# Performance work log

Hardware: AMD Instinct MI355X
Metric: run time of the kernel (lower is better)

The kernel has to match this reference:

```python
import jax, jax.numpy as jnp
import numpy as np

N_NODES = 100000
N_EDGES = 1600000
D_IN, D_HID, D_OUT = 64, 128, 64


def setup_inputs() -> dict:
    key = jax.random.key(0)
    ks = jax.random.split(key, 12)
    s = lambda d: 1.0 / np.sqrt(d)
    return {
        "x": jax.random.normal(ks[0], (N_NODES, D_IN), dtype=jnp.float32),
        "edge_index": jax.random.randint(ks[1], (2, N_EDGES), 0, N_NODES, dtype=jnp.int64),
        # conv1 MLP: Linear(D_IN->D_HID), ReLU, Linear(D_HID->D_HID)
        "W1a": jax.random.uniform(ks[2], (D_IN, D_HID), jnp.float32, -s(D_IN), s(D_IN)),
        "b1a": jnp.zeros((D_HID,), jnp.float32),
        "W1b": jax.random.uniform(ks[3], (D_HID, D_HID), jnp.float32, -s(D_HID), s(D_HID)),
        "b1b": jnp.zeros((D_HID,), jnp.float32),
        # conv2 MLP: Linear(D_HID->D_HID), ReLU, Linear(D_HID->D_HID)
        "W2a": jax.random.uniform(ks[4], (D_HID, D_HID), jnp.float32, -s(D_HID), s(D_HID)),
        "b2a": jnp.zeros((D_HID,), jnp.float32),
        "W2b": jax.random.uniform(ks[5], (D_HID, D_HID), jnp.float32, -s(D_HID), s(D_HID)),
        "b2b": jnp.zeros((D_HID,), jnp.float32),
        # final projection Linear(D_HID->D_OUT)
        "Wlin": jax.random.uniform(ks[6], (D_HID, D_OUT), jnp.float32, -s(D_HID), s(D_HID)),
        "blin": jnp.zeros((D_OUT,), jnp.float32),
    }


def _gin_conv(h, src, dst, Wa, ba, Wb, bb, num_nodes):
    # GINConv (eps=0): MLP((1+eps)*x + sum_{j->i} x_j)
    agg = jax.ops.segment_sum(h[src], dst, num_segments=num_nodes)  # [N, d]
    z = h + agg
    z = jax.nn.relu(z @ Wa + ba)
    return z @ Wb + bb


def reference(x, edge_index, W1a, b1a, W1b, b1b, W2a, b2a, W2b, b2b, Wlin, blin):
    n = x.shape[0]
    src, dst = edge_index[0], edge_index[1]
    h = jax.nn.relu(_gin_conv(x, src, dst, W1a, b1a, W1b, b1b, n))
    h = jax.nn.relu(_gin_conv(h, src, dst, W2a, b2a, W2b, b2b, n))
    return h @ Wlin + blin  # [N, D_OUT]
```

## Files before the change

### kernel.cpp

```cpp
#include <hip/hip_runtime.h>
#include <hip/hip_fp16.h>


typedef __attribute__((ext_vector_type(8))) short short8;
typedef __attribute__((ext_vector_type(8))) _Float16 half8;
typedef __attribute__((ext_vector_type(4))) float f32x4;
union F8 { unsigned u[4]; uint4 u4; short8 s; half8 h; };


constexpr int BUCKET_SHIFT = 9;
constexpr int BUCKET_NODES = 1 << BUCKET_SHIFT;
constexpr int CAP = 10240;
constexpr int EPB = 2048;
constexpr int NBUCK_MAX = 256;

__global__ __launch_bounds__(256) void prep_scatter_kernel(const int* __restrict__ ei, int E,
                                                           int* __restrict__ gcur,
                                                           int* __restrict__ gpk,
                                                           int nbuck, int nbs,
                                                           const float* __restrict__ W1a,
                                                           const float* __restrict__ W1b,
                                                           const float* __restrict__ W2a,
                                                           const float* __restrict__ W2b,
                                                           const float* __restrict__ Wlin,
                                                           short* __restrict__ hi,
                                                           const float* __restrict__ x,
                                                           __half2* __restrict__ x16, int n2,
                                                           int npb) {
    __shared__ int spk[EPB];
    __shared__ unsigned char sbuck[EPB];
    __shared__ int lcnt[NBUCK_MAX];
    __shared__ int lbase[NBUCK_MAX];
    __shared__ int lcur[NBUCK_MAX];
    __shared__ int gbase[NBUCK_MAX];
    __shared__ int stmp[256];

    const int t = threadIdx.x;

    if (blockIdx.x >= nbs) {
        int pb = blockIdx.x - nbs;
        int i = pb * 256 + t;
        if (i < 65536) {
            const float* W;
            int base, K, N;
            if (i < 8192)       { W = W1a;  base = 0;     K = 64;  N = 128; }
            else if (i < 24576) { W = W1b;  base = 8192;  K = 128; N = 128; }
            else if (i < 40960) { W = W2a;  base = 24576; K = 128; N = 128; }
            else if (i < 57344) { W = W2b;  base = 40960; K = 128; N = 128; }
            else                { W = Wlin; base = 57344; K = 128; N = 64;  }
            int rel = i - base;
            int NT = N >> 4;
            int j  = rel & 7;
            int l  = (rel >> 3) & 63;
            int tc = rel >> 9;
            int nt = tc % NT;
            int c  = tc / NT;
            int n  = nt * 16 + (l & 15);
            int k  = c * 32 + ((l >> 4) << 3) + j;
            float v = W[k * N + n];
            hi[i] = (short)__half_as_ushort(__float2half_rn(v));
        }
        for (int k = i; k < n2; k += npb * 256) {
            float2 v = reinterpret_cast<const float2*>(x)[k];
            x16[k] = __floats2half2_rn(v.x, v.y);
        }
        return;
    }

    const int e0 = blockIdx.x * EPB;
    const int ecnt = min(EPB, E - e0);

    for (int i = t; i < NBUCK_MAX; i += 256) lcnt[i] = 0;
    __syncthreads();

    for (int i = t; i < ecnt; i += 256) {
        int d = ei[E + e0 + i];
        atomicAdd(&lcnt[d >> BUCKET_SHIFT], 1);
    }
    __syncthreads();

    int v = lcnt[t];
    stmp[t] = v;
    __syncthreads();
    #pragma unroll
    for (int off = 1; off < 256; off <<= 1) {
        int add = (t >= off) ? stmp[t - off] : 0;
        __syncthreads();
        stmp[t] += add;
        __syncthreads();
    }
    lbase[t] = stmp[t] - v;
    lcur[t] = stmp[t] - v;
    __syncthreads();

    for (int i = t; i < ecnt; i += 256) {
        int s = ei[e0 + i];
        int d = ei[E + e0 + i];
        int b = d >> BUCKET_SHIFT;
        int p = atomicAdd(&lcur[b], 1);
        spk[p] = ((d & (BUCKET_NODES - 1)) << 17) | s;
        sbuck[p] = (unsigned char)b;
    }
    __syncthreads();

    if (t < nbuck) {
        int c = lcnt[t];
        gbase[t] = (c > 0) ? atomicAdd(&gcur[t], c) : 0;
    }
    __syncthreads();

    for (int i = t; i < ecnt; i += 256) {
        int b = sbuck[i];
        int gp = gbase[b] + (i - lbase[b]);
        if (gp < CAP) gpk[(size_t)b * CAP + gp] = spk[i];
    }
}

__global__ __launch_bounds__(1024) void bucket_build_kernel(const int* __restrict__ gpk,
                                                            const int* __restrict__ gcur,
                                                            int* __restrict__ row_start,
                                                            int* __restrict__ edge_src,
                                                            int N, int E, int nbuck) {
    __shared__ int h[BUCKET_NODES];
    __shared__ int s[BUCKET_NODES];
    __shared__ int sb[NBUCK_MAX];
    __shared__ int bbase_sh;
    const int t = threadIdx.x;
    const int b = blockIdx.x;
    const int base = b << BUCKET_SHIFT;

    if (t < NBUCK_MAX) {
        int c = 0;
        if (t < nbuck) c = min(gcur[t], CAP);
        sb[t] = c;
    }
    for (int i = t; i < BUCKET_NODES; i += 1024) h[i] = 0;
    __syncthreads();
    #pragma unroll
    for (int off = 1; off < NBUCK_MAX; off <<= 1) {
        int add = (t >= off && t < NBUCK_MAX) ? sb[t - off] : 0;
        __syncthreads();
        if (t < NBUCK_MAX) sb[t] += add;
        __syncthreads();
    }
    if (t == 0) {
        int cb0 = min(gcur[b], CAP);
        bbase_sh = sb[b] - cb0;
    }

    int cb = min(gcur[b], CAP);
    const int* pp = gpk + (size_t)b * CAP;
    for (int i = t; i < cb; i += 1024) atomicAdd(&h[((unsigned)pp[i]) >> 17], 1);
    __syncthreads();

    int c0 = (t < BUCKET_NODES) ? h[t] : 0;
    if (t < BUCKET_NODES) s[t] = c0;
    __syncthreads();
    #pragma unroll
    for (int off = 1; off < BUCKET_NODES; off <<= 1) {
        int add = (t >= off && t < BUCKET_NODES) ? s[t - off] : 0;
        __syncthreads();
        if (t < BUCKET_NODES) s[t] += add;
        __syncthreads();
    }
    if (t < BUCKET_NODES) {
        int ex = s[t] - c0 + bbase_sh;
        h[t] = ex;
        if (base + t < N) row_start[base + t] = ex;
    }
    if (b == 0 && t == 0) row_start[N] = E;
    __syncthreads();

    for (int i = t; i < cb; i += 1024) {
        unsigned pw = (unsigned)pp[i];
        int p = atomicAdd(&h[pw >> 17], 1);
        edge_src[p] = (int)(pw & 0x1FFFFu);
    }
}


__device__ inline void acc8(float* a, const uint4& v) {
    const __half2* h = reinterpret_cast<const __half2*>(&v);
    #pragma unroll
    for (int j = 0; j < 4; ++j) {
        float2 f = __half22float2(h[j]);
        a[2 * j]     += f.x;
        a[2 * j + 1] += f.y;
    }
}

__device__ inline uint4 pack8(const float* a) {
    uint4 o;
    __half2 h;
    h = __floats2half2_rn(a[0], a[1]); o.x = *reinterpret_cast<unsigned*>(&h);
    h = __floats2half2_rn(a[2], a[3]); o.y = *reinterpret_cast<unsigned*>(&h);
    h = __floats2half2_rn(a[4], a[5]); o.z = *reinterpret_cast<unsigned*>(&h);
    h = __floats2half2_rn(a[6], a[7]); o.w = *reinterpret_cast<unsigned*>(&h);
    return o;
}

__global__ __launch_bounds__(256) void agg128_fp16(const __half2* __restrict__ H16,
                                                   const int* __restrict__ row_start,
                                                   const int* __restrict__ edge_src,
                                                   __half2* __restrict__ Z16, int N) {
    int wave = threadIdx.x >> 6, lane = threadIdx.x & 63;
    int node = blockIdx.x * 4 + wave;
    if (node >= N) return;
    const int lg = lane >> 4;
    const int lo = lane & 15;
    const uint4* Hv = reinterpret_cast<const uint4*>(H16);
    int beg = row_start[node], end = row_start[node + 1];

    uint4 selfv = Hv[(size_t)node * 16 + lo];

    float a[8];
    #pragma unroll
    for (int j = 0; j < 8; ++j) a[j] = 0.f;
    if (lg == 0) acc8(a, selfv);

    int i = beg;
    for (; i + 16 <= end; i += 16) {
        int s0 = edge_src[i + lg];
        int s1 = edge_src[i + 4 + lg];
        int s2 = edge_src[i + 8 + lg];
        int s3 = edge_src[i + 12 + lg];
        uint4 v0 = Hv[(size_t)s0 * 16 + lo];
        uint4 v1 = Hv[(size_t)s1 * 16 + lo];
        uint4 v2 = Hv[(size_t)s2 * 16 + lo];
        uint4 v3 = Hv[(size_t)s3 * 16 + lo];
        acc8(a, v0); acc8(a, v1); acc8(a, v2); acc8(a, v3);
    }
    if (i + 8 <= end) {
        int s0 = edge_src[i + lg];
        int s1 = edge_src[i + 4 + lg];
        uint4 v0 = Hv[(size_t)s0 * 16 + lo];
        uint4 v1 = Hv[(size_t)s1 * 16 + lo];
        acc8(a, v0); acc8(a, v1);
        i += 8;
    }
    if (i + 4 <= end) {
        int s0 = edge_src[i + lg];
        uint4 v0 = Hv[(size_t)s0 * 16 + lo];
        acc8(a, v0);
        i += 4;
    }
    int rem = end - i;
    if (lg < rem) {
        int s0 = edge_src[i + lg];
        uint4 v0 = Hv[(size_t)s0 * 16 + lo];
        acc8(a, v0);
    }

    #pragma unroll
    for (int j = 0; j < 8; ++j) {
        a[j] += __shfl_xor(a[j], 16);
        a[j] += __shfl_xor(a[j], 32);
    }

    if (lg == 0) {
        reinterpret_cast<uint4*>(Z16)[(size_t)node * 16 + lo] = pack8(a);
    }
}

__global__ __launch_bounds__(256) void agg64_fp16(const __half2* __restrict__ H16,
                                                  const int* __restrict__ row_start,
                                                  const int* __restrict__ edge_src,
                                                  __half2* __restrict__ Z16, int N) {
    int wave = threadIdx.x >> 6, lane = threadIdx.x & 63;
    int node = blockIdx.x * 4 + wave;
    if (node >= N) return;
    const int lg = lane >> 3;
    const int lo = lane & 7;
    const uint4* Hv = reinterpret_cast<const uint4*>(H16);
    int beg = row_start[node], end = row_start[node + 1];

    uint4 selfv = Hv[(size_t)node * 8 + lo];

    float a[8];
    #pragma unroll
    for (int j = 0; j < 8; ++j) a[j] = 0.f;
    if (lg == 0) acc8(a, selfv);

    int i = beg;
    for (; i + 16 <= end; i += 16) {
        int s0 = edge_src[i + lg];
        int s1 = edge_src[i + 8 + lg];
        uint4 v0 = Hv[(size_t)s0 * 8 + lo];
        uint4 v1 = Hv[(size_t)s1 * 8 + lo];
        acc8(a, v0); acc8(a, v1);
    }
    if (i + 8 <= end) {
        int s0 = edge_src[i + lg];
        uint4 v0 = Hv[(size_t)s0 * 8 + lo];
        acc8(a, v0);
        i += 8;
    }
    int rem = end - i;
    if (lg < rem) {
        int s0 = edge_src[i + lg];
        uint4 v0 = Hv[(size_t)s0 * 8 + lo];
        acc8(a, v0);
    }

    #pragma unroll
    for (int j = 0; j < 8; ++j) {
        a[j] += __shfl_xor(a[j], 8);
        a[j] += __shfl_xor(a[j], 16);
        a[j] += __shfl_xor(a[j], 32);
    }

    if (lg == 0) {
        reinterpret_cast<uint4*>(Z16)[(size_t)node * 8 + lo] = pack8(a);
    }
}


template <int K, int NT>
__device__ inline void compute_directA(const __half2* __restrict__ z, int M, int m0,
                                       const short* __restrict__ WH,
                                       int w, int lane, f32x4 (*acc)[8]) {
    constexpr int KC = K / 32;
    const short8* bhp = reinterpret_cast<const short8*>(WH) + lane;
    const int q = lane >> 4, ln = lane & 15;
    const uint4* zr[2];
    #pragma unroll
    for (int mt = 0; mt < 2; ++mt) {
        int row = m0 + (w * 2 + mt) * 16 + ln;
        if (row >= M) row = M - 1;
        zr[mt] = reinterpret_cast<const uint4*>(z + (size_t)row * (K / 2));
    }
    for (int c = 0; c < KC; ++c) {
        F8 bh[NT];
        #pragma unroll
        for (int nt = 0; nt < NT; ++nt) bh[nt].s = bhp[(c * NT + nt) * 64];
        #pragma unroll
        for (int mt = 0; mt < 2; ++mt) {
            F8 ah;
            ah.u4 = zr[mt][c * 4 + q];
            #pragma unroll
            for (int nt = 0; nt < NT; ++nt) {
                acc[mt][nt] = __builtin_amdgcn_mfma_f32_16x16x32_f16(ah.h, bh[nt].h, acc[mt][nt], 0, 0, 0);
            }
        }
    }
}

template <int K, int NT>
__device__ inline void stage_compute(const unsigned* __restrict__ P,
                                     const short* __restrict__ WH,
                                     int w, int lane, f32x4 (*acc)[8]) {
    constexpr int KC = K / 32;
    const short8* bhp = reinterpret_cast<const short8*>(WH) + lane;
    for (int c = 0; c < KC; ++c) {
        F8 bh[NT];
        #pragma unroll
        for (int nt = 0; nt < NT; ++nt) {
            bh[nt].s = bhp[(c * NT + nt) * 64];
        }
        #pragma unroll
        for (int mt = 0; mt < 2; ++mt) {
            const int T = w * 2 + mt;
            const unsigned* Pb = P + ((T * KC + c) * 8) * 66 + lane;
            unsigned d[8];
            #pragma unroll
            for (int j = 0; j < 8; ++j) d[j] = Pb[j * 66];
            F8 ah;
            #pragma unroll
            for (int j = 0; j < 4; ++j) {
                ah.u[j] = __builtin_amdgcn_perm(d[2 * j + 1], d[2 * j], 0x05040100u);
            }
            #pragma unroll
            for (int nt = 0; nt < NT; ++nt) {
                acc[mt][nt] = __builtin_amdgcn_mfma_f32_16x16x32_f16(ah.h, bh[nt].h, acc[mt][nt], 0, 0, 0);
            }
        }
    }
}

__device__ inline void epilogue_tile(const f32x4* acc, const float* __restrict__ bias,
                                     unsigned* __restrict__ Pout, int T, int lane) {
    int q = lane >> 4, ln = lane & 15;
    #pragma unroll
    for (int nt = 0; nt < 8; ++nt) {
        int col = nt * 16 + ln;
        float b = bias[col];
        int c = col >> 5, jj = col & 7, q2 = (col >> 3) & 3;
        int pb = ((T * 4 + c) * 8 + jj) * 66;
        #pragma unroll
        for (int r = 0; r < 4; ++r) {
            float v = fmaxf(acc[nt][r] + b, 0.f);
            Pout[pb + ((q * 4 + r) | (q2 << 4))] =
                (unsigned)__half_as_ushort(__float2half_rn(v));
        }
    }
}

__global__ __launch_bounds__(256, 2) void mfma_mlp_A(const __half2* __restrict__ z16,
                                                     const short* __restrict__ WaH,
                                                     const float* __restrict__ ba,
                                                     const short* __restrict__ WbH,
                                                     const float* __restrict__ bb,
                                                     __half* __restrict__ H16out, int M) {
    __shared__ unsigned P[8 * 4 * 8 * 66];
    const int t = threadIdx.x;
    const int w = t >> 6, lane = t & 63;
    const int m0 = blockIdx.x * 128;
    const int q = lane >> 4, ln = lane & 15;

    f32x4 acc[2][8];
    #pragma unroll
    for (int mt = 0; mt < 2; ++mt)
        #pragma unroll
        for (int i = 0; i < 8; ++i) acc[mt][i] = (f32x4){0.f, 0.f, 0.f, 0.f};
    compute_directA<64, 8>(z16, M, m0, WaH, w, lane, acc);
    epilogue_tile(acc[0], ba, P, w * 2 + 0, lane);
    epilogue_tile(acc[1], ba, P, w * 2 + 1, lane);

    #pragma unroll
    for (int mt = 0; mt < 2; ++mt)
        #pragma unroll
        for (int i = 0; i < 8; ++i) acc[mt][i] = (f32x4){0.f, 0.f, 0.f, 0.f};
    stage_compute<128, 8>(P, WbH, w, lane, acc);

    #pragma unroll
    for (int mt = 0; mt < 2; ++mt) {
        #pragma unroll
        for (int nt = 0; nt < 8; ++nt) {
            int col = nt * 16 + ln;
            float b = bb[col];
            #pragma unroll
            for (int r = 0; r < 4; ++r) {
                int row = m0 + (w * 2 + mt) * 16 + q * 4 + r;
                if (row < M) {
                    float v = fmaxf(acc[mt][nt][r] + b, 0.f);
                    H16out[(size_t)row * 128 + col] = __float2half_rn(v);
                }
            }
        }
    }
}

__global__ __launch_bounds__(256, 2) void mfma_mlp_B(const __half2* __restrict__ z16,
                                                     const short* __restrict__ WaH,
                                                     const float* __restrict__ ba,
                                                     const short* __restrict__ WbH,
                                                     const float* __restrict__ bb,
                                                     const short* __restrict__ WlH,
                                                     const float* __restrict__ bl,
                                                     float* __restrict__ Out, int M) {
    __shared__ unsigned P[8 * 4 * 8 * 66];
    const int t = threadIdx.x;
    const int w = t >> 6, lane = t & 63;
    const int m0 = blockIdx.x * 128;
    const int q = lane >> 4, ln = lane & 15;

    f32x4 acc[2][8];
    #pragma unroll
    for (int mt = 0; mt < 2; ++mt)
        #pragma unroll
        for (int i = 0; i < 8; ++i) acc[mt][i] = (f32x4){0.f, 0.f, 0.f, 0.f};
    compute_directA<128, 8>(z16, M, m0, WaH, w, lane, acc);
    epilogue_tile(acc[0], ba, P, w * 2 + 0, lane);
    epilogue_tile(acc[1], ba, P, w * 2 + 1, lane);

    #pragma unroll
    for (int mt = 0; mt < 2; ++mt)
        #pragma unroll
        for (int i = 0; i < 8; ++i) acc[mt][i] = (f32x4){0.f, 0.f, 0.f, 0.f};
    stage_compute<128, 8>(P, WbH, w, lane, acc);
    epilogue_tile(acc[0], bb, P, w * 2 + 0, lane);
    epilogue_tile(acc[1], bb, P, w * 2 + 1, lane);

    #pragma unroll
    for (int mt = 0; mt < 2; ++mt)
        #pragma unroll
        for (int i = 0; i < 8; ++i) acc[mt][i] = (f32x4){0.f, 0.f, 0.f, 0.f};
    stage_compute<128, 4>(P, WlH, w, lane, acc);

    #pragma unroll
    for (int mt = 0; mt < 2; ++mt) {
        #pragma unroll
        for (int nt = 0; nt < 4; ++nt) {
            int col = nt * 16 + ln;
            float b = bl[col];
            #pragma unroll
            for (int r = 0; r < 4; ++r) {
                int row = m0 + (w * 2 + mt) * 16 + q * 4 + r;
                if (row < M) Out[(size_t)row * 64 + col] = acc[mt][nt][r] + b;
            }
        }
    }
}


extern "C" void kernel_launch(void* const* d_in, const int* in_sizes, int n_in,
                              void* d_out, int out_size, void* d_ws, size_t ws_size,
                              hipStream_t stream) {
    const float* x    = (const float*)d_in[0];
    const int*   ei   = (const int*)d_in[1];
    const float* W1a  = (const float*)d_in[2];
    const float* b1a  = (const float*)d_in[3];
    const float* W1b  = (const float*)d_in[4];
    const float* b1b  = (const float*)d_in[5];
    const float* W2a  = (const float*)d_in[6];
    const float* b2a  = (const float*)d_in[7];
    const float* W2b  = (const float*)d_in[8];
    const float* b2b  = (const float*)d_in[9];
    const float* Wlin = (const float*)d_in[10];
    const float* blin = (const float*)d_in[11];
    float* out = (float*)d_out;

    const int N = in_sizes[0] / 64;
    const int E = in_sizes[1] / 2;
    const int NBUCK = (N + BUCKET_NODES - 1) >> BUCKET_SHIFT;

    char* ws = (char*)d_ws;
    const size_t bufBytes = (size_t)N * 128 * sizeof(float);
    __half2* Zbuf = (__half2*)(ws + 0);
    char* B = ws + bufBytes;
    size_t off = 3 * bufBytes;
    int* row_start = (int*)(ws + off); off += ((size_t)(N + 1) * 4 + 15) & ~(size_t)15;
    int* cnt       = (int*)(ws + off); off += ((size_t)N * 4 + 15) & ~(size_t)15;
    int* partials  = (int*)(ws + off); off += 4096;
    int* gcur      = (int*)(ws + off); off += 4096;
    int* edge_src  = (int*)(ws + off); off += (size_t)E * 4;
    __half* h116   = (__half*)(ws + off); off += (size_t)N * 128 * 2;
    int* gpk = (int*)B;
    short* wHi = (short*)(B + (32u << 20));
    __half* x16 = (__half*)(B + (36u << 20));
    short* w1aH = wHi + 0;
    short* w1bH = wHi + 8192;
    short* w2aH = wHi + 24576;
    short* w2bH = wHi + 40960;
    short* wlH  = wHi + 57344;
    (void)cnt; (void)partials;

    const int NB_G = (N + 127) / 128;
    const int NB_S = (E + EPB - 1) / EPB;
    const int NB_A128 = (N + 3) / 4;
    const int NB_A64  = (N + 3) / 4;
    const int NB_P = 12500;

    hipMemsetAsync(gcur, 0, NBUCK_MAX * sizeof(int), stream);

    prep_scatter_kernel<<<NB_S + NB_P, 256, 0, stream>>>(ei, E, gcur, gpk, NBUCK, NB_S,
                                                         W1a, W1b, W2a, W2b, Wlin, wHi,
                                                         x, (__half2*)x16, N * 32, NB_P);

    bucket_build_kernel<<<NBUCK, 1024, 0, stream>>>(gpk, gcur, row_start, edge_src,
                                                    N, E, NBUCK);

    agg64_fp16<<<NB_A64, 256, 0, stream>>>((const __half2*)x16, row_start, edge_src, Zbuf, N);
    mfma_mlp_A<<<NB_G, 256, 0, stream>>>(Zbuf, w1aH, b1a, w1bH, b1b, h116, N);

    agg128_fp16<<<NB_A128, 256, 0, stream>>>((const __half2*)h116, row_start, edge_src, Zbuf, N);
    mfma_mlp_B<<<NB_G, 256, 0, stream>>>(Zbuf, w2aH, b2a, w2bH, b2b,
                                         wlH, blin, out, N);
}
```

Measured before the change: 306.6 us.

## Store MLP intermediate as packed fp16 in XOR-swizzled LDS tiles

The intermediate activations between the fused MLP layers were kept in LDS as one 32-bit word per fp16 value, so every MFMA A-fragment took eight scalar LDS reads and a perm step. They are now stored as packed halves in per-wave 16x136 tiles with an XOR swizzle on 8-element blocks. Each fragment then comes from a single 128-bit LDS read. LDS per block roughly halves, and launch bounds are raised to three blocks per SM to gain occupancy, at the cost of register pressure and possible spills.

```diff
diff --git a/kernel.cpp b/kernel.cpp
--- a/kernel.cpp
+++ b/kernel.cpp
@@ -315,6 +315,9 @@
 }
 
 
+constexpr int PROW = 136;
+constexpr int PREG = 16 * PROW;
+
 template <int K, int NT>
 __device__ inline void compute_directA(const __half2* __restrict__ z, int M, int m0,
                                        const short* __restrict__ WH,
@@ -345,30 +348,42 @@
     }
 }
 
-template <int K, int NT>
-__device__ inline void stage_compute(const unsigned* __restrict__ P,
-                                     const short* __restrict__ WH,
-                                     int w, int lane, f32x4 (*acc)[8]) {
-    constexpr int KC = K / 32;
+__device__ inline void epilogue16(const f32x4* acc, const float* __restrict__ bias,
+                                  __half* __restrict__ Pt, int lane) {
+    const int q = lane >> 4, ln = lane & 15;
+    #pragma unroll
+    for (int nt = 0; nt < 8; ++nt) {
+        int col = nt * 16 + ln;
+        float b = bias[col];
+        int cb = 2 * nt + (ln >> 3);
+        int pcol = (((cb ^ q) << 3) | (ln & 7));
+        #pragma unroll
+        for (int r = 0; r < 4; ++r) {
+            int row = q * 4 + r;
+            float v = fmaxf(acc[nt][r] + b, 0.f);
+            Pt[row * PROW + pcol] = __float2half_rn(v);
+        }
+    }
+}
+
+template <int NT>
+__device__ inline void computeP16(const __half* __restrict__ Pt0,
+                                  const __half* __restrict__ Pt1,
+                                  const short* __restrict__ WH,
+                                  int lane, f32x4 (*acc)[8]) {
     const short8* bhp = reinterpret_cast<const short8*>(WH) + lane;
-    for (int c = 0; c < KC; ++c) {
+    const int q = lane >> 4, ln = lane & 15;
+    const int key = (ln >> 2) & 3;
+    for (int c = 0; c < 4; ++c) {
         F8 bh[NT];
         #pragma unroll
-        for (int nt = 0; nt < NT; ++nt) {
-            bh[nt].s = bhp[(c * NT + nt) * 64];
-        }
+        for (int nt = 0; nt < NT; ++nt) bh[nt].s = bhp[(c * NT + nt) * 64];
         #pragma unroll
         for (int mt = 0; mt < 2; ++mt) {
-            const int T = w * 2 + mt;
-            const unsigned* Pb = P + ((T * KC + c) * 8) * 66 + lane;
-            unsigned d[8];
-            #pragma unroll
-            for (int j = 0; j < 8; ++j) d[j] = Pb[j * 66];
+            const __half* Pt = mt ? Pt1 : Pt0;
+            int blk = (c * 4 + q) ^ key;
             F8 ah;
-            #pragma unroll
-            for (int j = 0; j < 4; ++j) {
-                ah.u[j] = __builtin_amdgcn_perm(d[2 * j + 1], d[2 * j], 0x05040100u);
-            }
+            ah.u4 = *reinterpret_cast<const uint4*>(Pt + ln * PROW + blk * 8);
             #pragma unroll
             for (int nt = 0; nt < NT; ++nt) {
                 acc[mt][nt] = __builtin_amdgcn_mfma_f32_16x16x32_f16(ah.h, bh[nt].h, acc[mt][nt], 0, 0, 0);
@@ -377,35 +392,19 @@
     }
 }
 
-__device__ inline void epilogue_tile(const f32x4* acc, const float* __restrict__ bias,
-                                     unsigned* __restrict__ Pout, int T, int lane) {
-    int q = lane >> 4, ln = lane & 15;
-    #pragma unroll
-    for (int nt = 0; nt < 8; ++nt) {
-        int col = nt * 16 + ln;
-        float b = bias[col];
-        int c = col >> 5, jj = col & 7, q2 = (col >> 3) & 3;
-        int pb = ((T * 4 + c) * 8 + jj) * 66;
-        #pragma unroll
-        for (int r = 0; r < 4; ++r) {
-            float v = fmaxf(acc[nt][r] + b, 0.f);
-            Pout[pb + ((q * 4 + r) | (q2 << 4))] =
-                (unsigned)__half_as_ushort(__float2half_rn(v));
-        }
-    }
-}
-
-__global__ __launch_bounds__(256, 2) void mfma_mlp_A(const __half2* __restrict__ z16,
+__global__ __launch_bounds__(256, 3) void mfma_mlp_A(const __half2* __restrict__ z16,
                                                      const short* __restrict__ WaH,
                                                      const float* __restrict__ ba,
                                                      const short* __restrict__ WbH,
                                                      const float* __restrict__ bb,
                                                      __half* __restrict__ H16out, int M) {
-    __shared__ unsigned P[8 * 4 * 8 * 66];
+    __shared__ __half P16[8 * PREG];
     const int t = threadIdx.x;
     const int w = t >> 6, lane = t & 63;
     const int m0 = blockIdx.x * 128;
     const int q = lane >> 4, ln = lane & 15;
+    __half* Pt0 = P16 + (2 * w) * PREG;
+    __half* Pt1 = P16 + (2 * w + 1) * PREG;
 
     f32x4 acc[2][8];
     #pragma unroll
@@ -413,14 +412,14 @@
         #pragma unroll
         for (int i = 0; i < 8; ++i) acc[mt][i] = (f32x4){0.f, 0.f, 0.f, 0.f};
     compute_directA<64, 8>(z16, M, m0, WaH, w, lane, acc);
-    epilogue_tile(acc[0], ba, P, w * 2 + 0, lane);
-    epilogue_tile(acc[1], ba, P, w * 2 + 1, lane);
+    epilogue16(acc[0], ba, Pt0, lane);
+    epilogue16(acc[1], ba, Pt1, lane);
 
     #pragma unroll
     for (int mt = 0; mt < 2; ++mt)
         #pragma unroll
         for (int i = 0; i < 8; ++i) acc[mt][i] = (f32x4){0.f, 0.f, 0.f, 0.f};
-    stage_compute<128, 8>(P, WbH, w, lane, acc);
+    computeP16<8>(Pt0, Pt1, WbH, lane, acc);
 
     #pragma unroll
     for (int mt = 0; mt < 2; ++mt) {
@@ -440,7 +439,7 @@
     }
 }
 
-__global__ __launch_bounds__(256, 2) void mfma_mlp_B(const __half2* __restrict__ z16,
+__global__ __launch_bounds__(256, 3) void mfma_mlp_B(const __half2* __restrict__ z16,
                                                      const short* __restrict__ WaH,
                                                      const float* __restrict__ ba,
                                                      const short* __restrict__ WbH,
@@ -448,11 +447,13 @@
                                                      const short* __restrict__ WlH,
                                                      const float* __restrict__ bl,
                                                      float* __restrict__ Out, int M) {
-    __shared__ unsigned P[8 * 4 * 8 * 66];
+    __shared__ __half P16[8 * PREG];
     const int t = threadIdx.x;
     const int w = t >> 6, lane = t & 63;
     const int m0 = blockIdx.x * 128;
     const int q = lane >> 4, ln = lane & 15;
+    __half* Pt0 = P16 + (2 * w) * PREG;
+    __half* Pt1 = P16 + (2 * w + 1) * PREG;
 
     f32x4 acc[2][8];
     #pragma unroll
@@ -460,22 +461,22 @@
         #pragma unroll
         for (int i = 0; i < 8; ++i) acc[mt][i] = (f32x4){0.f, 0.f, 0.f, 0.f};
     compute_directA<128, 8>(z16, M, m0, WaH, w, lane, acc);
-    epilogue_tile(acc[0], ba, P, w * 2 + 0, lane);
-    epilogue_tile(acc[1], ba, P, w * 2 + 1, lane);
+    epilogue16(acc[0], ba, Pt0, lane);
+    epilogue16(acc[1], ba, Pt1, lane);
 
     #pragma unroll
     for (int mt = 0; mt < 2; ++mt)
         #pragma unroll
         for (int i = 0; i < 8; ++i) acc[mt][i] = (f32x4){0.f, 0.f, 0.f, 0.f};
-    stage_compute<128, 8>(P, WbH, w, lane, acc);
-    epilogue_tile(acc[0], bb, P, w * 2 + 0, lane);
-    epilogue_tile(acc[1], bb, P, w * 2 + 1, lane);
+    computeP16<8>(Pt0, Pt1, WbH, lane, acc);
+    epilogue16(acc[0], bb, Pt0, lane);
+    epilogue16(acc[1], bb, Pt1, lane);
 
     #pragma unroll
     for (int mt = 0; mt < 2; ++mt)
         #pragma unroll
         for (int i = 0; i < 8; ++i) acc[mt][i] = (f32x4){0.f, 0.f, 0.f, 0.f};
-    stage_compute<128, 4>(P, WlH, w, lane, acc);
+    computeP16<4>(Pt0, Pt1, WlH, lane, acc);
 
     #pragma unroll
     for (int mt = 0; mt < 2; ++mt) {
```

After: 312.9 us. 1.02x slower.
